# Optimization experiments

Measured on AMD Instinct MI355X. Metric: run time of the kernel, lower is better.

Reference implementation:

```python
import jax, jax.numpy as jnp
import numpy as np

H, W, C = 24, 8, 128
HW = H * W  # 192
EPS = 1e-5


def setup_inputs() -> dict:
    key = jax.random.key(0)
    k1, k2 = jax.random.split(key)
    P, G = 64, 64
    prob_fea = jax.random.normal(k1, (P, C, H, W), dtype=jnp.float32)
    gal_fea = jax.random.normal(k2, (G, C, H, W), dtype=jnp.float32)
    bn_gamma = jnp.ones((1,), jnp.float32)
    bn_beta = jnp.zeros((1,), jnp.float32)
    # reset_parameters: fc.weight filled with 1/(H*W)
    fc_w = jnp.full((1, 2 * HW), 1.0 / HW, dtype=jnp.float32)
    fc_b = jnp.zeros((1,), jnp.float32)
    lbn_gamma = jnp.ones((1,), jnp.float32)
    lbn_beta = jnp.zeros((1,), jnp.float32)
    return {"prob_fea": prob_fea, "gal_fea": gal_fea, "bn_gamma": bn_gamma,
            "bn_beta": bn_beta, "fc_w": fc_w, "fc_b": fc_b,
            "lbn_gamma": lbn_gamma, "lbn_beta": lbn_beta}


def reference(prob_fea, gal_fea, bn_gamma, bn_beta, fc_w, fc_b, lbn_gamma, lbn_beta):
    P = prob_fea.shape[0]
    G = gal_fea.shape[0]
    pf = prob_fea.reshape(P, C, HW)  # [P, C, hw]
    gf = gal_fea.reshape(G, C, HW)   # [G, C, hw]
    # all-pairs spatial correlation: score[p, g, r, s] = sum_c pf[p,c,s] * gf[g,c,r]
    score = jnp.einsum('pcs,gcr->pgrs', pf, gf)  # [P, G, hw, hw]
    max_r = jnp.max(score, axis=2)  # max over gallery positions r -> [P, G, hw]
    max_s = jnp.max(score, axis=3)  # max over probe positions s   -> [P, G, hw]
    feat = jnp.concatenate((max_r, max_s), axis=-1).reshape(-1, 2 * HW)  # [P*G, 2hw]
    # BatchNorm1d(1) on [N, 1, 2hw] in training mode: stats over all N*2hw elems
    mu = jnp.mean(feat)
    var = jnp.var(feat)
    feat = (feat - mu) * jax.lax.rsqrt(var + EPS) * bn_gamma[0] + bn_beta[0]
    # fc: [P*G, 2hw] @ [2hw, 1] + b
    logit = feat @ fc_w.T + fc_b  # [P*G, 1]
    # BatchNorm1d(1) on [N, 1]: stats over N
    lmu = jnp.mean(logit)
    lvar = jnp.var(logit)
    logit = (logit - lmu) * jax.lax.rsqrt(lvar + EPS) * lbn_gamma[0] + lbn_beta[0]
    return logit.reshape(P, G)
```

## Files before the change

### kernel.cpp

```cpp
#include <hip/hip_runtime.h>
#include <hip/hip_bf16.h>
#include <stdint.h>

#define HW 192
#define NC 128
#define KEPS 1e-5f
#define SLICE_B 49152

typedef __attribute__((ext_vector_type(8))) short short8;
typedef __attribute__((ext_vector_type(4))) float f32x4;

__device__ __forceinline__ float max3f(float a, float b, float c) {
  float d;
  asm("v_max3_f32 %0, %1, %2, %3" : "=v"(d) : "v"(a), "v"(b), "v"(c));
  return d;
}

__global__ __launch_bounds__(256)
void prep_kernel(const float* __restrict__ prob,
                 const float* __restrict__ gal,
                 char* __restrict__ probF,
                 char* __restrict__ galF) {
  __shared__ unsigned short lds[32 * 194];
  const int b = blockIdx.x;
  const int slice = b >> 2;
  const int ks = b & 3;
  const bool isProbe = (slice < 64);
  const float* src = isProbe ? prob + (size_t)slice * NC * HW
                             : gal + (size_t)(slice - 64) * NC * HW;
  char* dstBase = isProbe ? probF + (size_t)slice * SLICE_B
                          : galF + (size_t)(slice - 64) * SLICE_B;
  const float* s0 = src + (size_t)(ks * 32) * HW;
  #pragma unroll
  for (int k = 0; k < 24; ++k) {
    int i = k * 256 + threadIdx.x;
    int cp = i / HW;
    int hw = i - cp * HW;
    lds[cp * 194 + hw] =
        __builtin_bit_cast(unsigned short, __float2bfloat16(s0[i]));
  }
  __syncthreads();
  #pragma unroll
  for (int rep = 0; rep < 3; ++rep) {
    int idx = rep * 256 + threadIdx.x;
    int tile = idx >> 6;
    int lane = idx & 63;
    int q = lane >> 4;
    int r16 = lane & 15;
    int s = tile * 16 + r16;
    unsigned short v[8];
    #pragma unroll
    for (int j = 0; j < 8; ++j) v[j] = lds[(q * 8 + j) * 194 + s];
    short8 pack;
    #pragma unroll
    for (int j = 0; j < 8; ++j) pack[j] = (short)v[j];
    *(short8*)(dstBase + (((tile * 4 + ks) * 64 + lane) * 16)) = pack;
  }
}

template <int CTRL>
__device__ __forceinline__ float dpp_max(float x) {
  int xi = __builtin_bit_cast(int, x);
  int yi = __builtin_amdgcn_update_dpp(xi, xi, CTRL, 0xf, 0xf, false);
  return fmaxf(x, __builtin_bit_cast(float, yi));
}
__device__ __forceinline__ float ror16_max(float x) {
  x = dpp_max<0x121>(x);
  x = dpp_max<0x122>(x);
  x = dpp_max<0x124>(x);
  x = dpp_max<0x128>(x);
  return x;
}

__global__ __launch_bounds__(256, 3)
void pair_kernel(const char* __restrict__ galF,
                 const char* __restrict__ probF,
                 const float* __restrict__ fc_w,
                 float* __restrict__ Wout,
                 float* __restrict__ sPart,
                 float* __restrict__ qPart) {
  __shared__ float cmP[2][4][192];
  __shared__ float rmF[2][192];
  __shared__ float red[2][4];
  __shared__ float red2[8];

  const int tid = threadIdx.x;
  const int lane = tid & 63;
  const int wid = tid >> 6;
  const int q = lane >> 4;
  const int r16 = lane & 15;

  const int g = blockIdx.x >> 5;
  const int pc = blockIdx.x & 31;

  const char* gB = galF + (size_t)g * SLICE_B + lane * 16;
  short8 a[3][4];
  #pragma unroll
  for (int m = 0; m < 3; ++m)
    #pragma unroll
    for (int ks = 0; ks < 4; ++ks)
      a[m][ks] = *(const short8*)(gB + (((wid * 3 + m) * 4 + ks) * 1024));

  const float w0 = fc_w[tid];
  const float w1 = (tid < 128) ? fc_w[256 + tid] : 0.f;

  float s_acc = 0.f, q_acc = 0.f;
  const f32x4 zz = (f32x4){0.f, 0.f, 0.f, 0.f};

  #pragma unroll 1
  for (int pi = 0; pi < 2; ++pi) {
    const char* pB = probF + (size_t)(pc * 2 + pi) * SLICE_B + lane * 16;
    float rm[3][4];

    #pragma unroll 1
    for (int qt = 0; qt < 4; ++qt) {
      f32x4 acc[3][3];
      __builtin_amdgcn_s_setprio(1);
      #pragma unroll
      for (int nt = 0; nt < 3; ++nt) {
        const char* bb = pB + ((qt * 3 + nt) * 4) * 1024;
        short8 b0 = *(const short8*)(bb);
        short8 b1 = *(const short8*)(bb + 1024);
        short8 b2 = *(const short8*)(bb + 2048);
        short8 b3 = *(const short8*)(bb + 3072);
        #pragma unroll
        for (int m = 0; m < 3; ++m)
          acc[m][nt] = __builtin_amdgcn_mfma_f32_16x16x32_bf16(a[m][0], b0, zz, 0, 0, 0);
        #pragma unroll
        for (int m = 0; m < 3; ++m)
          acc[m][nt] = __builtin_amdgcn_mfma_f32_16x16x32_bf16(a[m][1], b1, acc[m][nt], 0, 0, 0);
        #pragma unroll
        for (int m = 0; m < 3; ++m)
          acc[m][nt] = __builtin_amdgcn_mfma_f32_16x16x32_bf16(a[m][2], b2, acc[m][nt], 0, 0, 0);
        #pragma unroll
        for (int m = 0; m < 3; ++m)
          acc[m][nt] = __builtin_amdgcn_mfma_f32_16x16x32_bf16(a[m][3], b3, acc[m][nt], 0, 0, 0);
      }
      __builtin_amdgcn_s_setprio(0);

      #pragma unroll
      for (int nt = 0; nt < 3; ++nt) {
        float m0 = max3f(acc[0][nt][0], acc[0][nt][1], acc[0][nt][2]);
        float m1 = max3f(acc[0][nt][3], acc[1][nt][0], acc[1][nt][1]);
        float m2 = max3f(acc[1][nt][2], acc[1][nt][3], acc[2][nt][0]);
        float m3 = max3f(acc[2][nt][1], acc[2][nt][2], acc[2][nt][3]);
        float cm = max3f(m0, m1, m2);
        cm = fmaxf(cm, m3);
        cm = fmaxf(cm, __shfl_xor(cm, 16));
        cm = fmaxf(cm, __shfl_xor(cm, 32));
        if (lane < 16) cmP[pi][wid][qt * 48 + nt * 16 + r16] = cm;
      }
      #pragma unroll
      for (int m = 0; m < 3; ++m)
        #pragma unroll
        for (int j = 0; j < 4; ++j) {
          float v = max3f(acc[m][0][j], acc[m][1][j], acc[m][2][j]);
          rm[m][j] = (qt == 0) ? v : fmaxf(rm[m][j], v);
        }
    }
    #pragma unroll
    for (int m = 0; m < 3; ++m)
      #pragma unroll
      for (int j = 0; j < 4; ++j) {
        float v = ror16_max(rm[m][j]);
        if (r16 == j) rmF[pi][wid * 48 + m * 16 + q * 4 + j] = v;
      }
  }

  __syncthreads();

  #pragma unroll
  for (int pi = 0; pi < 2; ++pi) {
    float v;
    if (tid < 192) {
      float c01 = fmaxf(cmP[pi][0][tid], cmP[pi][1][tid]);
      v = max3f(c01, cmP[pi][2][tid], cmP[pi][3][tid]);
    } else {
      v = rmF[pi][tid - 192];
    }
    s_acc += v; q_acc += v * v;
    float w = v * w0;
    if (tid < 128) {
      float v1 = rmF[pi][tid + 64];
      s_acc += v1; q_acc += v1 * v1;
      w += v1 * w1;
    }
    #pragma unroll
    for (int msk = 1; msk < 64; msk <<= 1) w += __shfl_xor(w, msk);
    if (lane == 0) red[pi][wid] = w;
  }
  #pragma unroll
  for (int msk = 1; msk < 64; msk <<= 1) {
    s_acc += __shfl_xor(s_acc, msk);
    q_acc += __shfl_xor(q_acc, msk);
  }
  if (lane == 0) { red2[wid] = s_acc; red2[4 + wid] = q_acc; }
  __syncthreads();
  if (tid < 2)
    Wout[(pc * 2 + tid) * 64 + g] =
        red[tid][0] + red[tid][1] + red[tid][2] + red[tid][3];
  if (tid == 0) {
    sPart[blockIdx.x] = red2[0] + red2[1] + red2[2] + red2[3];
    qPart[blockIdx.x] = red2[4] + red2[5] + red2[6] + red2[7];
  }
}

__device__ __forceinline__ float block_sum(float v, float* rbuf, float* bc, int nw) {
  int t = threadIdx.x, lane = t & 63, wid = t >> 6;
  #pragma unroll
  for (int m = 1; m < 64; m <<= 1) v += __shfl_xor(v, m);
  if (lane == 0) rbuf[wid] = v;
  __syncthreads();
  if (t == 0) {
    float r = 0.f;
    for (int i = 0; i < nw; ++i) r += rbuf[i];
    bc[0] = r;
  }
  __syncthreads();
  float res = bc[0];
  __syncthreads();
  return res;
}

__global__ __launch_bounds__(1024)
void finalize_kernel(const float* __restrict__ Wv,
                     const float* __restrict__ sPart,
                     const float* __restrict__ qPart,
                     const float* __restrict__ fc_w,
                     const float* __restrict__ fc_b,
                     const float* __restrict__ bn_g,
                     const float* __restrict__ bn_b,
                     const float* __restrict__ lbn_g,
                     const float* __restrict__ lbn_b,
                     float* __restrict__ out) {
  __shared__ float rbuf[16];
  __shared__ float bc[1];
  const int t = threadIdx.x;

  float S = block_sum(sPart[t] + sPart[t + 1024], rbuf, bc, 16);
  float Q = block_sum(qPart[t] + qPart[t + 1024], rbuf, bc, 16);
  float SW = block_sum((t < 384) ? fc_w[t] : 0.f, rbuf, bc, 16);

  const float Nf = 4096.0f * 384.0f;
  float mu = S / Nf;
  float var = Q / Nf - mu * mu;
  float istd = rsqrtf(var + KEPS);
  float cA = istd * bn_g[0];
  float off = bn_b[0] * SW + fc_b[0] - cA * mu * SW;

  float l[4];
  float ls = 0.f;
  #pragma unroll
  for (int i = 0; i < 4; ++i) {
    int n = t + i * 1024;
    l[i] = cA * Wv[n] + off;
    ls += l[i];
  }
  float LS = block_sum(ls, rbuf, bc, 16);
  float lmu = LS / 4096.0f;
  float lq = 0.f;
  #pragma unroll
  for (int i = 0; i < 4; ++i) { float d = l[i] - lmu; lq += d * d; }
  float LQ = block_sum(lq, rbuf, bc, 16);
  float lvar = LQ / 4096.0f;
  float sc = lbn_g[0] * rsqrtf(lvar + KEPS);
  float lb = lbn_b[0];
  #pragma unroll
  for (int i = 0; i < 4; ++i) {
    int n = t + i * 1024;
    out[n] = (l[i] - lmu) * sc + lb;
  }
}

extern "C" void kernel_launch(void* const* d_in, const int* in_sizes, int n_in,
                              void* d_out, int out_size, void* d_ws, size_t ws_size,
                              hipStream_t stream) {
  const float* prob  = (const float*)d_in[0];
  const float* gal   = (const float*)d_in[1];
  const float* bn_g  = (const float*)d_in[2];
  const float* bn_b  = (const float*)d_in[3];
  const float* fc_w  = (const float*)d_in[4];
  const float* fc_b  = (const float*)d_in[5];
  const float* lbn_g = (const float*)d_in[6];
  const float* lbn_b = (const float*)d_in[7];
  float* out = (float*)d_out;

  char* ws = (char*)d_ws;
  char* probF = ws;
  char* galF  = ws + 3145728;
  float* Wv    = (float*)(ws + 6291456);
  float* sPart = (float*)(ws + 6307840);
  float* qPart = (float*)(ws + 6316032);

  prep_kernel<<<512, 256, 0, stream>>>(prob, gal, probF, galF);
  pair_kernel<<<2048, 256, 0, stream>>>(galF, probF, fc_w, Wv, sPart, qPart);
  finalize_kernel<<<1, 1024, 0, stream>>>(Wv, sPart, qPart, fc_w, fc_b,
                                          bn_g, bn_b, lbn_g, lbn_b, out);
}
```

Before: 59.22 us.

## Double-buffer probe tiles in LDS via async global-to-LDS loads

Probe B-operand tiles now stream into a double-buffered LDS region using global_load_lds, with the next chunk prefetched while MFMAs run on the current one. The pair loop is flattened into eight steps, and the first probe's reduction and Wout store are interleaved into the second probe's iterations. Occupancy hint rises from 3 to 4 blocks per SM. The goal is to hide global load latency, at the cost of 24KB extra LDS, two barriers per step, and possible register pressure under the higher occupancy bound.

```diff
diff --git a/kernel.cpp b/kernel.cpp
--- a/kernel.cpp
+++ b/kernel.cpp
@@ -6,6 +6,7 @@
 #define NC 128
 #define KEPS 1e-5f
 #define SLICE_B 49152
+#define QTB 12288
 
 typedef __attribute__((ext_vector_type(8))) short short8;
 typedef __attribute__((ext_vector_type(4))) float f32x4;
@@ -46,16 +47,19 @@
     int tile = idx >> 6;
     int lane = idx & 63;
     int q = lane >> 4;
-    int r16 = lane & 15;
-    int s = tile * 16 + r16;
-    unsigned short v[8];
-    #pragma unroll
-    for (int j = 0; j < 8; ++j) v[j] = lds[(q * 8 + j) * 194 + s];
+    int s = tile * 16 + (lane & 15);
     short8 pack;
     #pragma unroll
-    for (int j = 0; j < 8; ++j) pack[j] = (short)v[j];
+    for (int j = 0; j < 8; ++j)
+      pack[j] = (short)lds[(q * 8 + j) * 194 + s];
     *(short8*)(dstBase + (((tile * 4 + ks) * 64 + lane) * 16)) = pack;
   }
+}
+
+__device__ __forceinline__ void gl_lds16(const void* gsrc, void* ldst) {
+  __builtin_amdgcn_global_load_lds(
+      (const __attribute__((address_space(1))) void*)gsrc,
+      (__attribute__((address_space(3))) void*)ldst, 16, 0, 0);
 }
 
 template <int CTRL>
@@ -72,16 +76,17 @@
   return x;
 }
 
-__global__ __launch_bounds__(256, 3)
+__global__ __launch_bounds__(256, 4)
 void pair_kernel(const char* __restrict__ galF,
                  const char* __restrict__ probF,
                  const float* __restrict__ fc_w,
                  float* __restrict__ Wout,
                  float* __restrict__ sPart,
                  float* __restrict__ qPart) {
+  __shared__ char buf[2][QTB];
   __shared__ float cmP[2][4][192];
   __shared__ float rmF[2][192];
-  __shared__ float red[2][4];
+  __shared__ float redp[2][4];
   __shared__ float red2[8];
 
   const int tid = threadIdx.x;
@@ -104,90 +109,135 @@
   const float w0 = fc_w[tid];
   const float w1 = (tid < 128) ? fc_w[256 + tid] : 0.f;
 
+  const char* pBase = probF + (size_t)(pc * 2) * SLICE_B;
+
+  #pragma unroll
+  for (int c = 0; c < 3; ++c)
+    gl_lds16(pBase + (wid * 3 + c) * 1024 + lane * 16,
+             &buf[0][(wid * 3 + c) * 1024]);
+
+  float rm[3][4];
   float s_acc = 0.f, q_acc = 0.f;
   const f32x4 zz = (f32x4){0.f, 0.f, 0.f, 0.f};
 
-  #pragma unroll 1
-  for (int pi = 0; pi < 2; ++pi) {
-    const char* pB = probF + (size_t)(pc * 2 + pi) * SLICE_B + lane * 16;
-    float rm[3][4];
-
-    #pragma unroll 1
-    for (int qt = 0; qt < 4; ++qt) {
-      f32x4 acc[3][3];
-      __builtin_amdgcn_s_setprio(1);
-      #pragma unroll
-      for (int nt = 0; nt < 3; ++nt) {
-        const char* bb = pB + ((qt * 3 + nt) * 4) * 1024;
-        short8 b0 = *(const short8*)(bb);
-        short8 b1 = *(const short8*)(bb + 1024);
-        short8 b2 = *(const short8*)(bb + 2048);
-        short8 b3 = *(const short8*)(bb + 3072);
-        #pragma unroll
-        for (int m = 0; m < 3; ++m)
-          acc[m][nt] = __builtin_amdgcn_mfma_f32_16x16x32_bf16(a[m][0], b0, zz, 0, 0, 0);
-        #pragma unroll
-        for (int m = 0; m < 3; ++m)
-          acc[m][nt] = __builtin_amdgcn_mfma_f32_16x16x32_bf16(a[m][1], b1, acc[m][nt], 0, 0, 0);
-        #pragma unroll
-        for (int m = 0; m < 3; ++m)
-          acc[m][nt] = __builtin_amdgcn_mfma_f32_16x16x32_bf16(a[m][2], b2, acc[m][nt], 0, 0, 0);
-        #pragma unroll
-        for (int m = 0; m < 3; ++m)
-          acc[m][nt] = __builtin_amdgcn_mfma_f32_16x16x32_bf16(a[m][3], b3, acc[m][nt], 0, 0, 0);
+  for (int t = 0; t < 8; ++t) {
+    const int qc = t & 3;
+    const int pi = t >> 2;
+
+    if (t + 1 < 8) {
+      const char* src = pBase + (size_t)((t + 1) >> 2) * SLICE_B
+                        + ((t + 1) & 3) * QTB;
+      char* dst = buf[(t + 1) & 1];
+      #pragma unroll
+      for (int c = 0; c < 3; ++c)
+        gl_lds16(src + (wid * 3 + c) * 1024 + lane * 16,
+                 dst + (wid * 3 + c) * 1024);
+      asm volatile("s_waitcnt vmcnt(3)" ::: "memory");
+    } else {
+      asm volatile("s_waitcnt vmcnt(0)" ::: "memory");
+    }
+    __builtin_amdgcn_sched_barrier(0);
+    __builtin_amdgcn_s_barrier();
+    const char* cur = buf[t & 1];
+
+    if (t == 4) {
+      float v;
+      if (tid < 192) {
+        float c01 = fmaxf(cmP[0][0][tid], cmP[0][1][tid]);
+        v = max3f(c01, cmP[0][2][tid], cmP[0][3][tid]);
+      } else {
+        v = rmF[0][tid - 192];
       }
-      __builtin_amdgcn_s_setprio(0);
-
-      #pragma unroll
-      for (int nt = 0; nt < 3; ++nt) {
-        float m0 = max3f(acc[0][nt][0], acc[0][nt][1], acc[0][nt][2]);
-        float m1 = max3f(acc[0][nt][3], acc[1][nt][0], acc[1][nt][1]);
-        float m2 = max3f(acc[1][nt][2], acc[1][nt][3], acc[2][nt][0]);
-        float m3 = max3f(acc[2][nt][1], acc[2][nt][2], acc[2][nt][3]);
-        float cm = max3f(m0, m1, m2);
-        cm = fmaxf(cm, m3);
-        cm = fmaxf(cm, __shfl_xor(cm, 16));
-        cm = fmaxf(cm, __shfl_xor(cm, 32));
-        if (lane < 16) cmP[pi][wid][qt * 48 + nt * 16 + r16] = cm;
+      s_acc += v; q_acc += v * v;
+      float w = v * w0;
+      if (tid < 128) {
+        float v1 = rmF[0][tid + 64];
+        s_acc += v1; q_acc += v1 * v1;
+        w += v1 * w1;
       }
+      #pragma unroll
+      for (int msk = 1; msk < 64; msk <<= 1) w += __shfl_xor(w, msk);
+      if (lane == 0) redp[0][wid] = w;
+    }
+    if (t == 5 && tid == 0)
+      Wout[(pc * 2) * 64 + g] = redp[0][0] + redp[0][1] + redp[0][2] + redp[0][3];
+
+    __builtin_amdgcn_s_setprio(1);
+    f32x4 acc[3][3];
+    #pragma unroll
+    for (int nt = 0; nt < 3; ++nt) {
+      const char* bb = cur + nt * 4096 + lane * 16;
+      short8 b0 = *(const short8*)(bb);
+      short8 b1 = *(const short8*)(bb + 1024);
+      short8 b2 = *(const short8*)(bb + 2048);
+      short8 b3 = *(const short8*)(bb + 3072);
+      #pragma unroll
+      for (int m = 0; m < 3; ++m)
+        acc[m][nt] = __builtin_amdgcn_mfma_f32_16x16x32_bf16(a[m][0], b0, zz, 0, 0, 0);
+      #pragma unroll
+      for (int m = 0; m < 3; ++m)
+        acc[m][nt] = __builtin_amdgcn_mfma_f32_16x16x32_bf16(a[m][1], b1, acc[m][nt], 0, 0, 0);
+      #pragma unroll
+      for (int m = 0; m < 3; ++m)
+        acc[m][nt] = __builtin_amdgcn_mfma_f32_16x16x32_bf16(a[m][2], b2, acc[m][nt], 0, 0, 0);
+      #pragma unroll
+      for (int m = 0; m < 3; ++m)
+        acc[m][nt] = __builtin_amdgcn_mfma_f32_16x16x32_bf16(a[m][3], b3, acc[m][nt], 0, 0, 0);
+    }
+    __builtin_amdgcn_s_setprio(0);
+
+    #pragma unroll
+    for (int nt = 0; nt < 3; ++nt) {
+      float m0 = max3f(acc[0][nt][0], acc[0][nt][1], acc[0][nt][2]);
+      float m1 = max3f(acc[0][nt][3], acc[1][nt][0], acc[1][nt][1]);
+      float m2 = max3f(acc[1][nt][2], acc[1][nt][3], acc[2][nt][0]);
+      float m3 = max3f(acc[2][nt][1], acc[2][nt][2], acc[2][nt][3]);
+      float cm = max3f(m0, m1, m2);
+      cm = fmaxf(cm, m3);
+      cm = fmaxf(cm, __shfl_xor(cm, 16));
+      cm = fmaxf(cm, __shfl_xor(cm, 32));
+      if (lane < 16) cmP[pi][wid][qc * 48 + nt * 16 + r16] = cm;
+    }
+    #pragma unroll
+    for (int m = 0; m < 3; ++m)
+      #pragma unroll
+      for (int j = 0; j < 4; ++j) {
+        float v = max3f(acc[m][0][j], acc[m][1][j], acc[m][2][j]);
+        rm[m][j] = (qc == 0) ? v : fmaxf(rm[m][j], v);
+      }
+    if (qc == 3) {
       #pragma unroll
       for (int m = 0; m < 3; ++m)
         #pragma unroll
         for (int j = 0; j < 4; ++j) {
-          float v = max3f(acc[m][0][j], acc[m][1][j], acc[m][2][j]);
-          rm[m][j] = (qt == 0) ? v : fmaxf(rm[m][j], v);
+          float v = ror16_max(rm[m][j]);
+          if (r16 == j) rmF[pi][wid * 48 + m * 16 + q * 4 + j] = v;
         }
     }
-    #pragma unroll
-    for (int m = 0; m < 3; ++m)
-      #pragma unroll
-      for (int j = 0; j < 4; ++j) {
-        float v = ror16_max(rm[m][j]);
-        if (r16 == j) rmF[pi][wid * 48 + m * 16 + q * 4 + j] = v;
-      }
-  }
-
-  __syncthreads();
-
-  #pragma unroll
-  for (int pi = 0; pi < 2; ++pi) {
+
+    asm volatile("s_waitcnt lgkmcnt(0)" ::: "memory");
+    __builtin_amdgcn_sched_barrier(0);
+    __builtin_amdgcn_s_barrier();
+  }
+
+  {
     float v;
     if (tid < 192) {
-      float c01 = fmaxf(cmP[pi][0][tid], cmP[pi][1][tid]);
-      v = max3f(c01, cmP[pi][2][tid], cmP[pi][3][tid]);
+      float c01 = fmaxf(cmP[1][0][tid], cmP[1][1][tid]);
+      v = max3f(c01, cmP[1][2][tid], cmP[1][3][tid]);
     } else {
-      v = rmF[pi][tid - 192];
+      v = rmF[1][tid - 192];
     }
     s_acc += v; q_acc += v * v;
     float w = v * w0;
     if (tid < 128) {
-      float v1 = rmF[pi][tid + 64];
+      float v1 = rmF[1][tid + 64];
       s_acc += v1; q_acc += v1 * v1;
       w += v1 * w1;
     }
     #pragma unroll
     for (int msk = 1; msk < 64; msk <<= 1) w += __shfl_xor(w, msk);
-    if (lane == 0) red[pi][wid] = w;
+    if (lane == 0) redp[1][wid] = w;
   }
   #pragma unroll
   for (int msk = 1; msk < 64; msk <<= 1) {
@@ -196,10 +246,8 @@
   }
   if (lane == 0) { red2[wid] = s_acc; red2[4 + wid] = q_acc; }
   __syncthreads();
-  if (tid < 2)
-    Wout[(pc * 2 + tid) * 64 + g] =
-        red[tid][0] + red[tid][1] + red[tid][2] + red[tid][3];
   if (tid == 0) {
+    Wout[(pc * 2 + 1) * 64 + g] = redp[1][0] + redp[1][1] + redp[1][2] + redp[1][3];
     sPart[blockIdx.x] = red2[0] + red2[1] + red2[2] + red2[3];
     qPart[blockIdx.x] = red2[4] + red2[5] + red2[6] + red2[7];
   }
```

New measurement: 60.13 us. No clear change (+1.5%).

## Software-pipeline probe tile loads and MFMA with max reduction in pair kernel

Applied to the files above, without the earlier changes.

Replaces the per-qt loop in pair_kernel with a fully unrolled, manually pipelined sequence over the 12 probe column groups. It triple-buffers the B-operand global loads and double-buffers accumulators, so the column/row max reduction of one group overlaps the MFMAs of the next. Occupancy hint drops from 3 to 2 waves-per-SIMD blocks to give room for the extra registers. The risk is lower latency hiding from reduced occupancy and register pressure from the extra live buffers.

```diff
diff --git a/kernel.cpp b/kernel.cpp
--- a/kernel.cpp
+++ b/kernel.cpp
@@ -46,14 +46,11 @@
     int tile = idx >> 6;
     int lane = idx & 63;
     int q = lane >> 4;
-    int r16 = lane & 15;
-    int s = tile * 16 + r16;
-    unsigned short v[8];
-    #pragma unroll
-    for (int j = 0; j < 8; ++j) v[j] = lds[(q * 8 + j) * 194 + s];
+    int s = tile * 16 + (lane & 15);
     short8 pack;
     #pragma unroll
-    for (int j = 0; j < 8; ++j) pack[j] = (short)v[j];
+    for (int j = 0; j < 8; ++j)
+      pack[j] = (short)lds[(q * 8 + j) * 194 + s];
     *(short8*)(dstBase + (((tile * 4 + ks) * 64 + lane) * 16)) = pack;
   }
 }
@@ -72,7 +69,7 @@
   return x;
 }
 
-__global__ __launch_bounds__(256, 3)
+__global__ __launch_bounds__(256, 2)
 void pair_kernel(const char* __restrict__ galF,
                  const char* __restrict__ probF,
                  const float* __restrict__ fc_w,
@@ -111,53 +108,101 @@
   for (int pi = 0; pi < 2; ++pi) {
     const char* pB = probF + (size_t)(pc * 2 + pi) * SLICE_B + lane * 16;
     float rm[3][4];
-
-    #pragma unroll 1
-    for (int qt = 0; qt < 4; ++qt) {
-      f32x4 acc[3][3];
-      __builtin_amdgcn_s_setprio(1);
+    #pragma unroll
+    for (int m = 0; m < 3; ++m)
       #pragma unroll
-      for (int nt = 0; nt < 3; ++nt) {
-        const char* bb = pB + ((qt * 3 + nt) * 4) * 1024;
-        short8 b0 = *(const short8*)(bb);
-        short8 b1 = *(const short8*)(bb + 1024);
-        short8 b2 = *(const short8*)(bb + 2048);
-        short8 b3 = *(const short8*)(bb + 3072);
-        #pragma unroll
-        for (int m = 0; m < 3; ++m)
-          acc[m][nt] = __builtin_amdgcn_mfma_f32_16x16x32_bf16(a[m][0], b0, zz, 0, 0, 0);
-        #pragma unroll
-        for (int m = 0; m < 3; ++m)
-          acc[m][nt] = __builtin_amdgcn_mfma_f32_16x16x32_bf16(a[m][1], b1, acc[m][nt], 0, 0, 0);
-        #pragma unroll
-        for (int m = 0; m < 3; ++m)
-          acc[m][nt] = __builtin_amdgcn_mfma_f32_16x16x32_bf16(a[m][2], b2, acc[m][nt], 0, 0, 0);
-        #pragma unroll
-        for (int m = 0; m < 3; ++m)
-          acc[m][nt] = __builtin_amdgcn_mfma_f32_16x16x32_bf16(a[m][3], b3, acc[m][nt], 0, 0, 0);
-      }
-      __builtin_amdgcn_s_setprio(0);
-
-      #pragma unroll
-      for (int nt = 0; nt < 3; ++nt) {
-        float m0 = max3f(acc[0][nt][0], acc[0][nt][1], acc[0][nt][2]);
-        float m1 = max3f(acc[0][nt][3], acc[1][nt][0], acc[1][nt][1]);
-        float m2 = max3f(acc[1][nt][2], acc[1][nt][3], acc[2][nt][0]);
-        float m3 = max3f(acc[2][nt][1], acc[2][nt][2], acc[2][nt][3]);
-        float cm = max3f(m0, m1, m2);
-        cm = fmaxf(cm, m3);
-        cm = fmaxf(cm, __shfl_xor(cm, 16));
-        cm = fmaxf(cm, __shfl_xor(cm, 32));
-        if (lane < 16) cmP[pi][wid][qt * 48 + nt * 16 + r16] = cm;
-      }
-      #pragma unroll
-      for (int m = 0; m < 3; ++m)
-        #pragma unroll
-        for (int j = 0; j < 4; ++j) {
-          float v = max3f(acc[m][0][j], acc[m][1][j], acc[m][2][j]);
-          rm[m][j] = (qt == 0) ? v : fmaxf(rm[m][j], v);
-        }
-    }
+      for (int j = 0; j < 4; ++j) rm[m][j] = -1e30f;
+
+    short8 b00, b01, b02, b03;
+    short8 b10, b11, b12, b13;
+    short8 b20, b21, b22, b23;
+    f32x4 aA0, aA1, aA2;
+    f32x4 aB0, aB1, aB2;
+
+#define LOADQ(Q0, Q1, Q2, Q3, GRP) do {                         \
+    const char* bb_ = pB + (GRP) * 4096;                        \
+    Q0 = *(const short8*)(bb_);                                 \
+    Q1 = *(const short8*)(bb_ + 1024);                          \
+    Q2 = *(const short8*)(bb_ + 2048);                          \
+    Q3 = *(const short8*)(bb_ + 3072);                          \
+  } while (0)
+
+#define MFMA_G(A0, A1, A2, Q0, Q1, Q2, Q3) do {                              \
+    A0 = __builtin_amdgcn_mfma_f32_16x16x32_bf16(a[0][0], Q0, zz, 0, 0, 0);  \
+    A1 = __builtin_amdgcn_mfma_f32_16x16x32_bf16(a[1][0], Q0, zz, 0, 0, 0);  \
+    A2 = __builtin_amdgcn_mfma_f32_16x16x32_bf16(a[2][0], Q0, zz, 0, 0, 0);  \
+    A0 = __builtin_amdgcn_mfma_f32_16x16x32_bf16(a[0][1], Q1, A0, 0, 0, 0);  \
+    A1 = __builtin_amdgcn_mfma_f32_16x16x32_bf16(a[1][1], Q1, A1, 0, 0, 0);  \
+    A2 = __builtin_amdgcn_mfma_f32_16x16x32_bf16(a[2][1], Q1, A2, 0, 0, 0);  \
+    A0 = __builtin_amdgcn_mfma_f32_16x16x32_bf16(a[0][2], Q2, A0, 0, 0, 0);  \
+    A1 = __builtin_amdgcn_mfma_f32_16x16x32_bf16(a[1][2], Q2, A1, 0, 0, 0);  \
+    A2 = __builtin_amdgcn_mfma_f32_16x16x32_bf16(a[2][2], Q2, A2, 0, 0, 0);  \
+    A0 = __builtin_amdgcn_mfma_f32_16x16x32_bf16(a[0][3], Q3, A0, 0, 0, 0);  \
+    A1 = __builtin_amdgcn_mfma_f32_16x16x32_bf16(a[1][3], Q3, A1, 0, 0, 0);  \
+    A2 = __builtin_amdgcn_mfma_f32_16x16x32_bf16(a[2][3], Q3, A2, 0, 0, 0);  \
+  } while (0)
+
+#define REDUCE_G(A0, A1, A2, GRP) do {                                       \
+    float m0_ = max3f(A0[0], A0[1], A0[2]);                                  \
+    float m1_ = max3f(A0[3], A1[0], A1[1]);                                  \
+    float m2_ = max3f(A1[2], A1[3], A2[0]);                                  \
+    float m3_ = max3f(A2[1], A2[2], A2[3]);                                  \
+    float cm_ = fmaxf(max3f(m0_, m1_, m2_), m3_);                            \
+    cm_ = fmaxf(cm_, __shfl_xor(cm_, 16));                                   \
+    cm_ = fmaxf(cm_, __shfl_xor(cm_, 32));                                   \
+    if (lane < 16) cmP[pi][wid][(GRP) * 16 + r16] = cm_;                     \
+    rm[0][0] = fmaxf(rm[0][0], A0[0]); rm[0][1] = fmaxf(rm[0][1], A0[1]);    \
+    rm[0][2] = fmaxf(rm[0][2], A0[2]); rm[0][3] = fmaxf(rm[0][3], A0[3]);    \
+    rm[1][0] = fmaxf(rm[1][0], A1[0]); rm[1][1] = fmaxf(rm[1][1], A1[1]);    \
+    rm[1][2] = fmaxf(rm[1][2], A1[2]); rm[1][3] = fmaxf(rm[1][3], A1[3]);    \
+    rm[2][0] = fmaxf(rm[2][0], A2[0]); rm[2][1] = fmaxf(rm[2][1], A2[1]);    \
+    rm[2][2] = fmaxf(rm[2][2], A2[2]); rm[2][3] = fmaxf(rm[2][3], A2[3]);    \
+  } while (0)
+
+    LOADQ(b00, b01, b02, b03, 0);
+    LOADQ(b10, b11, b12, b13, 1);
+
+    __builtin_amdgcn_s_setprio(1);
+    LOADQ(b20, b21, b22, b23, 2);
+    MFMA_G(aA0, aA1, aA2, b00, b01, b02, b03);
+    LOADQ(b00, b01, b02, b03, 3);
+    MFMA_G(aB0, aB1, aB2, b10, b11, b12, b13);
+    REDUCE_G(aA0, aA1, aA2, 0);
+    LOADQ(b10, b11, b12, b13, 4);
+    MFMA_G(aA0, aA1, aA2, b20, b21, b22, b23);
+    REDUCE_G(aB0, aB1, aB2, 1);
+    LOADQ(b20, b21, b22, b23, 5);
+    MFMA_G(aB0, aB1, aB2, b00, b01, b02, b03);
+    REDUCE_G(aA0, aA1, aA2, 2);
+    LOADQ(b00, b01, b02, b03, 6);
+    MFMA_G(aA0, aA1, aA2, b10, b11, b12, b13);
+    REDUCE_G(aB0, aB1, aB2, 3);
+    LOADQ(b10, b11, b12, b13, 7);
+    MFMA_G(aB0, aB1, aB2, b20, b21, b22, b23);
+    REDUCE_G(aA0, aA1, aA2, 4);
+    LOADQ(b20, b21, b22, b23, 8);
+    MFMA_G(aA0, aA1, aA2, b00, b01, b02, b03);
+    REDUCE_G(aB0, aB1, aB2, 5);
+    LOADQ(b00, b01, b02, b03, 9);
+    MFMA_G(aB0, aB1, aB2, b10, b11, b12, b13);
+    REDUCE_G(aA0, aA1, aA2, 6);
+    LOADQ(b10, b11, b12, b13, 10);
+    MFMA_G(aA0, aA1, aA2, b20, b21, b22, b23);
+    REDUCE_G(aB0, aB1, aB2, 7);
+    LOADQ(b20, b21, b22, b23, 11);
+    MFMA_G(aB0, aB1, aB2, b00, b01, b02, b03);
+    REDUCE_G(aA0, aA1, aA2, 8);
+    MFMA_G(aA0, aA1, aA2, b10, b11, b12, b13);
+    REDUCE_G(aB0, aB1, aB2, 9);
+    MFMA_G(aB0, aB1, aB2, b20, b21, b22, b23);
+    REDUCE_G(aA0, aA1, aA2, 10);
+    REDUCE_G(aB0, aB1, aB2, 11);
+    __builtin_amdgcn_s_setprio(0);
+
+#undef LOADQ
+#undef MFMA_G
+#undef REDUCE_G
+
     #pragma unroll
     for (int m = 0; m < 3; ++m)
       #pragma unroll
```

Result: faster. 57.74 us, median of 3 (-2.5%).

## Process two gallery items per block to share probe fragment loads

Applied to the files above, without the earlier changes.

Each block of the pair kernel now holds A fragments for two gallery samples in registers and loops over one probe sample. Every probe B fragment load then feeds twice as many MFMAs, and the two accumulator sets are interleaved so independent MFMA chains can overlap. This doubles register use for A fragments and accumulators, so launch bounds drop from 3 to 2 blocks per CU, trading occupancy for reuse. The prep kernel loop is also simplified, which does not change the work done.

```diff
diff --git a/kernel.cpp b/kernel.cpp
--- a/kernel.cpp
+++ b/kernel.cpp
@@ -46,14 +46,11 @@
     int tile = idx >> 6;
     int lane = idx & 63;
     int q = lane >> 4;
-    int r16 = lane & 15;
-    int s = tile * 16 + r16;
-    unsigned short v[8];
-    #pragma unroll
-    for (int j = 0; j < 8; ++j) v[j] = lds[(q * 8 + j) * 194 + s];
+    int s = tile * 16 + (lane & 15);
     short8 pack;
     #pragma unroll
-    for (int j = 0; j < 8; ++j) pack[j] = (short)v[j];
+    for (int j = 0; j < 8; ++j)
+      pack[j] = (short)lds[(q * 8 + j) * 194 + s];
     *(short8*)(dstBase + (((tile * 4 + ks) * 64 + lane) * 16)) = pack;
   }
 }
@@ -72,7 +69,7 @@
   return x;
 }
 
-__global__ __launch_bounds__(256, 3)
+__global__ __launch_bounds__(256, 2)
 void pair_kernel(const char* __restrict__ galF,
                  const char* __restrict__ probF,
                  const float* __restrict__ fc_w,
@@ -90,104 +87,134 @@
   const int q = lane >> 4;
   const int r16 = lane & 15;
 
-  const int g = blockIdx.x >> 5;
-  const int pc = blockIdx.x & 31;
-
-  const char* gB = galF + (size_t)g * SLICE_B + lane * 16;
-  short8 a[3][4];
+  const int p = blockIdx.x >> 5;
+  const int gp = blockIdx.x & 31;
+
+  const char* g0B = galF + (size_t)(2 * gp) * SLICE_B + lane * 16;
+  const char* g1B = galF + (size_t)(2 * gp + 1) * SLICE_B + lane * 16;
+  short8 a0[3][4], a1[3][4];
   #pragma unroll
   for (int m = 0; m < 3; ++m)
     #pragma unroll
-    for (int ks = 0; ks < 4; ++ks)
-      a[m][ks] = *(const short8*)(gB + (((wid * 3 + m) * 4 + ks) * 1024));
+    for (int ks = 0; ks < 4; ++ks) {
+      a0[m][ks] = *(const short8*)(g0B + (((wid * 3 + m) * 4 + ks) * 1024));
+      a1[m][ks] = *(const short8*)(g1B + (((wid * 3 + m) * 4 + ks) * 1024));
+    }
 
   const float w0 = fc_w[tid];
   const float w1 = (tid < 128) ? fc_w[256 + tid] : 0.f;
 
+  const char* pB = probF + (size_t)p * SLICE_B + lane * 16;
+
+  float rm0[3][4], rm1[3][4];
   float s_acc = 0.f, q_acc = 0.f;
   const f32x4 zz = (f32x4){0.f, 0.f, 0.f, 0.f};
 
   #pragma unroll 1
-  for (int pi = 0; pi < 2; ++pi) {
-    const char* pB = probF + (size_t)(pc * 2 + pi) * SLICE_B + lane * 16;
-    float rm[3][4];
-
-    #pragma unroll 1
-    for (int qt = 0; qt < 4; ++qt) {
-      f32x4 acc[3][3];
-      __builtin_amdgcn_s_setprio(1);
-      #pragma unroll
-      for (int nt = 0; nt < 3; ++nt) {
-        const char* bb = pB + ((qt * 3 + nt) * 4) * 1024;
-        short8 b0 = *(const short8*)(bb);
-        short8 b1 = *(const short8*)(bb + 1024);
-        short8 b2 = *(const short8*)(bb + 2048);
-        short8 b3 = *(const short8*)(bb + 3072);
-        #pragma unroll
-        for (int m = 0; m < 3; ++m)
-          acc[m][nt] = __builtin_amdgcn_mfma_f32_16x16x32_bf16(a[m][0], b0, zz, 0, 0, 0);
-        #pragma unroll
-        for (int m = 0; m < 3; ++m)
-          acc[m][nt] = __builtin_amdgcn_mfma_f32_16x16x32_bf16(a[m][1], b1, acc[m][nt], 0, 0, 0);
-        #pragma unroll
-        for (int m = 0; m < 3; ++m)
-          acc[m][nt] = __builtin_amdgcn_mfma_f32_16x16x32_bf16(a[m][2], b2, acc[m][nt], 0, 0, 0);
-        #pragma unroll
-        for (int m = 0; m < 3; ++m)
-          acc[m][nt] = __builtin_amdgcn_mfma_f32_16x16x32_bf16(a[m][3], b3, acc[m][nt], 0, 0, 0);
-      }
-      __builtin_amdgcn_s_setprio(0);
-
-      #pragma unroll
-      for (int nt = 0; nt < 3; ++nt) {
-        float m0 = max3f(acc[0][nt][0], acc[0][nt][1], acc[0][nt][2]);
-        float m1 = max3f(acc[0][nt][3], acc[1][nt][0], acc[1][nt][1]);
-        float m2 = max3f(acc[1][nt][2], acc[1][nt][3], acc[2][nt][0]);
-        float m3 = max3f(acc[2][nt][1], acc[2][nt][2], acc[2][nt][3]);
-        float cm = max3f(m0, m1, m2);
-        cm = fmaxf(cm, m3);
+  for (int qt = 0; qt < 4; ++qt) {
+    f32x4 acc0[3][3], acc1[3][3];
+    __builtin_amdgcn_s_setprio(1);
+    #pragma unroll
+    for (int nt = 0; nt < 3; ++nt) {
+      const char* bb = pB + ((qt * 3 + nt) * 4) * 1024;
+      short8 b0 = *(const short8*)(bb);
+      short8 b1 = *(const short8*)(bb + 1024);
+      short8 b2 = *(const short8*)(bb + 2048);
+      short8 b3 = *(const short8*)(bb + 3072);
+      #pragma unroll
+      for (int m = 0; m < 3; ++m)
+        acc0[m][nt] = __builtin_amdgcn_mfma_f32_16x16x32_bf16(a0[m][0], b0, zz, 0, 0, 0);
+      #pragma unroll
+      for (int m = 0; m < 3; ++m)
+        acc1[m][nt] = __builtin_amdgcn_mfma_f32_16x16x32_bf16(a1[m][0], b0, zz, 0, 0, 0);
+      #pragma unroll
+      for (int m = 0; m < 3; ++m)
+        acc0[m][nt] = __builtin_amdgcn_mfma_f32_16x16x32_bf16(a0[m][1], b1, acc0[m][nt], 0, 0, 0);
+      #pragma unroll
+      for (int m = 0; m < 3; ++m)
+        acc1[m][nt] = __builtin_amdgcn_mfma_f32_16x16x32_bf16(a1[m][1], b1, acc1[m][nt], 0, 0, 0);
+      #pragma unroll
+      for (int m = 0; m < 3; ++m)
+        acc0[m][nt] = __builtin_amdgcn_mfma_f32_16x16x32_bf16(a0[m][2], b2, acc0[m][nt], 0, 0, 0);
+      #pragma unroll
+      for (int m = 0; m < 3; ++m)
+        acc1[m][nt] = __builtin_amdgcn_mfma_f32_16x16x32_bf16(a1[m][2], b2, acc1[m][nt], 0, 0, 0);
+      #pragma unroll
+      for (int m = 0; m < 3; ++m)
+        acc0[m][nt] = __builtin_amdgcn_mfma_f32_16x16x32_bf16(a0[m][3], b3, acc0[m][nt], 0, 0, 0);
+      #pragma unroll
+      for (int m = 0; m < 3; ++m)
+        acc1[m][nt] = __builtin_amdgcn_mfma_f32_16x16x32_bf16(a1[m][3], b3, acc1[m][nt], 0, 0, 0);
+    }
+    __builtin_amdgcn_s_setprio(0);
+
+    #pragma unroll
+    for (int nt = 0; nt < 3; ++nt) {
+      {
+        float m0 = max3f(acc0[0][nt][0], acc0[0][nt][1], acc0[0][nt][2]);
+        float m1 = max3f(acc0[0][nt][3], acc0[1][nt][0], acc0[1][nt][1]);
+        float m2 = max3f(acc0[1][nt][2], acc0[1][nt][3], acc0[2][nt][0]);
+        float m3 = max3f(acc0[2][nt][1], acc0[2][nt][2], acc0[2][nt][3]);
+        float cm = fmaxf(max3f(m0, m1, m2), m3);
         cm = fmaxf(cm, __shfl_xor(cm, 16));
         cm = fmaxf(cm, __shfl_xor(cm, 32));
-        if (lane < 16) cmP[pi][wid][qt * 48 + nt * 16 + r16] = cm;
+        if (lane < 16) cmP[0][wid][qt * 48 + nt * 16 + r16] = cm;
       }
-      #pragma unroll
-      for (int m = 0; m < 3; ++m)
-        #pragma unroll
-        for (int j = 0; j < 4; ++j) {
-          float v = max3f(acc[m][0][j], acc[m][1][j], acc[m][2][j]);
-          rm[m][j] = (qt == 0) ? v : fmaxf(rm[m][j], v);
-        }
+      {
+        float m0 = max3f(acc1[0][nt][0], acc1[0][nt][1], acc1[0][nt][2]);
+        float m1 = max3f(acc1[0][nt][3], acc1[1][nt][0], acc1[1][nt][1]);
+        float m2 = max3f(acc1[1][nt][2], acc1[1][nt][3], acc1[2][nt][0]);
+        float m3 = max3f(acc1[2][nt][1], acc1[2][nt][2], acc1[2][nt][3]);
+        float cm = fmaxf(max3f(m0, m1, m2), m3);
+        cm = fmaxf(cm, __shfl_xor(cm, 16));
+        cm = fmaxf(cm, __shfl_xor(cm, 32));
+        if (lane < 16) cmP[1][wid][qt * 48 + nt * 16 + r16] = cm;
+      }
     }
     #pragma unroll
     for (int m = 0; m < 3; ++m)
       #pragma unroll
       for (int j = 0; j < 4; ++j) {
-        float v = ror16_max(rm[m][j]);
-        if (r16 == j) rmF[pi][wid * 48 + m * 16 + q * 4 + j] = v;
+        float v0 = max3f(acc0[m][0][j], acc0[m][1][j], acc0[m][2][j]);
+        float v1 = max3f(acc1[m][0][j], acc1[m][1][j], acc1[m][2][j]);
+        rm0[m][j] = (qt == 0) ? v0 : fmaxf(rm0[m][j], v0);
+        rm1[m][j] = (qt == 0) ? v1 : fmaxf(rm1[m][j], v1);
       }
   }
 
-  __syncthreads();
-
-  #pragma unroll
-  for (int pi = 0; pi < 2; ++pi) {
+  #pragma unroll
+  for (int m = 0; m < 3; ++m)
+    #pragma unroll
+    for (int j = 0; j < 4; ++j) {
+      float v0 = ror16_max(rm0[m][j]);
+      float v1 = ror16_max(rm1[m][j]);
+      if (r16 == j) {
+        rmF[0][wid * 48 + m * 16 + q * 4 + j] = v0;
+        rmF[1][wid * 48 + m * 16 + q * 4 + j] = v1;
+      }
+    }
+
+  __syncthreads();
+
+  #pragma unroll
+  for (int gi = 0; gi < 2; ++gi) {
     float v;
     if (tid < 192) {
-      float c01 = fmaxf(cmP[pi][0][tid], cmP[pi][1][tid]);
-      v = max3f(c01, cmP[pi][2][tid], cmP[pi][3][tid]);
+      float c01 = fmaxf(cmP[gi][0][tid], cmP[gi][1][tid]);
+      v = max3f(c01, cmP[gi][2][tid], cmP[gi][3][tid]);
     } else {
-      v = rmF[pi][tid - 192];
+      v = rmF[gi][tid - 192];
     }
     s_acc += v; q_acc += v * v;
     float w = v * w0;
     if (tid < 128) {
-      float v1 = rmF[pi][tid + 64];
+      float v1 = rmF[gi][tid + 64];
       s_acc += v1; q_acc += v1 * v1;
       w += v1 * w1;
     }
     #pragma unroll
     for (int msk = 1; msk < 64; msk <<= 1) w += __shfl_xor(w, msk);
-    if (lane == 0) red[pi][wid] = w;
+    if (lane == 0) red[gi][wid] = w;
   }
   #pragma unroll
   for (int msk = 1; msk < 64; msk <<= 1) {
@@ -197,7 +224,7 @@
   if (lane == 0) { red2[wid] = s_acc; red2[4 + wid] = q_acc; }
   __syncthreads();
   if (tid < 2)
-    Wout[(pc * 2 + tid) * 64 + g] =
+    Wout[p * 64 + 2 * gp + tid] =
         red[tid][0] + red[tid][1] + red[tid][2] + red[tid][3];
   if (tid == 0) {
     sPart[blockIdx.x] = red2[0] + red2[1] + red2[2] + red2[3];
```

New measurement: 70.87 us. 19.7% more time.
